# Optimization experiments

Measured on AMD Instinct MI355X. Metric: run time of the kernel, lower is better.

The kernel has to match this reference:

```python
import jax, jax.numpy as jnp
import numpy as np

DEC = 1024
MEM = 1024


def setup_inputs() -> dict:
    key = jax.random.key(0)
    k1, k2, k3, k4, k5 = jax.random.split(key, 5)
    decoder_state = jax.random.normal(k1, (64, DEC), dtype=jnp.float32)
    memory_bank = jax.random.normal(k2, (64, 2048, MEM), dtype=jnp.float32)
    src_mask = jnp.ones((64, 2048), dtype=jnp.int32)
    # learned params (torch Linear: y = x @ W.T); store as (in, out) for einsum
    s = 1.0 / np.sqrt(DEC)
    W_v = jax.random.uniform(k3, (DEC,), jnp.float32, -s, s)            # v: decoder_size -> 1
    W_dec = jax.random.uniform(k4, (DEC, DEC), jnp.float32, -s, s)       # decode_project
    sm = 1.0 / np.sqrt(MEM)
    W_mem = jax.random.uniform(k5, (MEM, DEC), jnp.float32, -sm, sm)     # memory_project
    return {"decoder_state": decoder_state, "memory_bank": memory_bank,
            "src_mask": src_mask, "W_v": W_v, "W_dec": W_dec, "W_mem": W_mem}


def reference(decoder_state, memory_bank, src_mask, W_v, W_dec, W_mem):
    # encoder_feature: [B,S,D]; dec_feature: [B,D]
    enc_feat = jnp.einsum('bsm,md->bsd', memory_bank, W_mem)
    dec_feat = jnp.einsum('bm,md->bd', decoder_state, W_dec)
    e = jnp.tanh(enc_feat + dec_feat[:, None, :])      # [B,S,D]
    scores = jnp.einsum('bsd,d->bs', e, W_v)           # [B,S]
    scores = jnp.where(src_mask == 0, -jnp.inf, scores)
    attn_dist = jax.nn.softmax(scores, axis=-1)        # [B,S]
    context = jnp.einsum('bs,bsm->bm', attn_dist, memory_bank)  # [B,M]
    return (context, attn_dist)
```

## Files before the change

### kernel.cpp

```cpp
#include <hip/hip_runtime.h>

typedef __bf16 bf16;
typedef __bf16 bf16x8 __attribute__((ext_vector_type(8)));
typedef float f32x4 __attribute__((ext_vector_type(4)));

constexpr int kB = 64;
constexpr int kS = 2048;
constexpr int kD = 1024;
constexpr int kM = 1024;
constexpr int kRows = kB * kS;

__device__ __forceinline__ void async_copy16(const void* gsrc, void* ldst) {
    __builtin_amdgcn_global_load_lds(
        (const __attribute__((address_space(1))) void*)gsrc,
        (__attribute__((address_space(3))) void*)ldst, 16, 0, 0);
}

__device__ __forceinline__ float fast_tanh(float x) {
    float e = __expf(2.0f * x);
    return 1.0f - 2.0f * __builtin_amdgcn_rcpf(e + 1.0f);
}

__global__ __launch_bounds__(256) void wmem_transpose_kernel(
    const float* __restrict__ Wm, bf16* __restrict__ WT) {
    __shared__ bf16 tile[64][72];
    const int d0 = (blockIdx.x & 15) * 64;
    const int m0 = (blockIdx.x >> 4) * 64;
    const int lane = threadIdx.x & 63;
    const int grp  = threadIdx.x >> 6;
    #pragma unroll
    for (int r = 0; r < 16; ++r) {
        const int m = m0 + grp * 16 + r;
        tile[lane][grp * 16 + r] = (bf16)Wm[m * 1024 + d0 + lane];
    }
    __syncthreads();
    #pragma unroll
    for (int r = 0; r < 16; ++r) {
        const int d = d0 + grp * 16 + r;
        WT[d * 1024 + m0 + lane] = tile[grp * 16 + r][lane];
    }
}

__global__ __launch_bounds__(256) void dec_project_kernel(
    const float* __restrict__ dec, const float* __restrict__ Wd,
    float* __restrict__ decf) {
    const int b = blockIdx.x;
    const int d = blockIdx.y * 256 + threadIdx.x;
    const float* drow = dec + b * kD;
    float acc = 0.f;
    #pragma unroll 8
    for (int m = 0; m < kM; ++m)
        acc += drow[m] * Wd[(size_t)m * kD + d];
    decf[b * kD + d] = acc;
}

constexpr int BM = 128, BN = 256, BK = 32, APAD = 40;
constexpr int NCOL = kD / BN;
constexpr int NSTEP = kM / BK;

__global__ __launch_bounds__(512, 4) void attn_scores_kernel(
    const float* __restrict__ MBank,
    const bf16*  __restrict__ WT,
    const float* __restrict__ decf,
    const float* __restrict__ Wv,
    float* __restrict__ spart)
{
    __shared__ bf16 Abuf[2][BM * APAD];
    __shared__ bf16 Bbuf[2][BN * BK];
    __shared__ float sred[BM * 4];

    const int tid  = threadIdx.x;
    const int wave = tid >> 6;
    const int lane = tid & 63;
    const int ln   = lane & 15;
    const int quad = lane >> 4;

    const int L = blockIdx.y * NCOL + blockIdx.x;
    const int jw = L >> 3;
    const int rowTile = ((L & 7) << 7) + (jw >> 2);
    const int colTile = jw & 3;
    const int R0 = rowTile * BM;
    const int C0 = colTile * BN;
    const int batch = rowTile >> 4;

    const int wr = (wave >> 2) * 64;
    const int wc = (wave & 3) * 64;

    const int arow  = tid >> 2;
    const int akseg = (tid & 3) * 8;
    const float* aptr = MBank + (size_t)(R0 + arow) * kM + akseg;

    const int bn0   = (lane >> 2);
    const int bkoff = (lane & 3) * 8;

    {
        const float* ap = aptr;
        f32x4 v0 = *(const f32x4*)(ap + 0);
        f32x4 v1 = *(const f32x4*)(ap + 4);
        #pragma unroll
        for (int jj = 0; jj < 2; ++jj) {
            const int chunk = wave * 2 + jj;
            const int n = chunk * 16 + bn0;
            async_copy16(WT + (size_t)(C0 + n) * kM + bkoff,
                         Bbuf[0] + chunk * 512);
        }
        bf16x8 w0;
        w0[0]=(bf16)v0[0]; w0[1]=(bf16)v0[1]; w0[2]=(bf16)v0[2]; w0[3]=(bf16)v0[3];
        w0[4]=(bf16)v1[0]; w0[5]=(bf16)v1[1]; w0[6]=(bf16)v1[2]; w0[7]=(bf16)v1[3];
        *(bf16x8*)(Abuf[0] + arow * APAD + akseg) = w0;
    }
    __syncthreads();

    f32x4 acc[4][4];
    const f32x4 zero = {0.f, 0.f, 0.f, 0.f};
    #pragma unroll
    for (int i = 0; i < 4; ++i)
        #pragma unroll
        for (int j = 0; j < 4; ++j)
            acc[i][j] = zero;

    #pragma unroll 2
    for (int t = 0; t < NSTEP; ++t) {
        const int cur = t & 1, nxt = cur ^ 1;
        const bool pf = (t + 1 < NSTEP);
        const int k1 = (t + 1) * BK;

        f32x4 v0, v1;
        if (pf) {
            const float* ap = aptr + k1;
            v0 = *(const f32x4*)(ap + 0);
            v1 = *(const f32x4*)(ap + 4);
            #pragma unroll
            for (int jj = 0; jj < 2; ++jj) {
                const int chunk = wave * 2 + jj;
                const int n = chunk * 16 + bn0;
                async_copy16(WT + (size_t)(C0 + n) * kM + k1 + bkoff,
                             Bbuf[nxt] + chunk * 512);
            }
        }

        const bf16* Ac = Abuf[cur];
        const bf16* Bc = Bbuf[cur];
        bf16x8 af[4], bfr[4];
        #pragma unroll
        for (int i = 0; i < 4; ++i)
            af[i] = *(const bf16x8*)(Ac + (wr + i * 16 + ln) * APAD + quad * 8);
        #pragma unroll
        for (int j = 0; j < 4; ++j)
            bfr[j] = *(const bf16x8*)(Bc + (wc + j * 16 + ln) * BK + quad * 8);
        __builtin_amdgcn_s_setprio(1);
        #pragma unroll
        for (int i = 0; i < 4; ++i)
            #pragma unroll
            for (int j = 0; j < 4; ++j)
                acc[i][j] = __builtin_amdgcn_mfma_f32_16x16x32_bf16(
                    af[i], bfr[j], acc[i][j], 0, 0, 0);
        __builtin_amdgcn_s_setprio(0);

        if (pf) {
            bf16x8 w0;
            w0[0]=(bf16)v0[0]; w0[1]=(bf16)v0[1]; w0[2]=(bf16)v0[2]; w0[3]=(bf16)v0[3];
            w0[4]=(bf16)v1[0]; w0[5]=(bf16)v1[1]; w0[6]=(bf16)v1[2]; w0[7]=(bf16)v1[3];
            *(bf16x8*)(Abuf[nxt] + arow * APAD + akseg) = w0;
        }
        __syncthreads();
    }

    float wv[4], df[4];
    #pragma unroll
    for (int j = 0; j < 4; ++j) {
        const int d = C0 + wc + j * 16 + ln;
        wv[j] = Wv[d];
        df[j] = decf[batch * kD + d];
    }
    float rp[4][4];
    #pragma unroll
    for (int i = 0; i < 4; ++i) {
        #pragma unroll
        for (int r = 0; r < 4; ++r) {
            float p = 0.f;
            #pragma unroll
            for (int j = 0; j < 4; ++j) {
                float x = acc[i][j][r] + df[j];
                p += fast_tanh(x) * wv[j];
            }
            #pragma unroll
            for (int off = 1; off < 16; off <<= 1)
                p += __shfl_xor(p, off, 64);
            rp[i][r] = p;
        }
    }
    if (ln == 0) {
        #pragma unroll
        for (int i = 0; i < 4; ++i)
            #pragma unroll
            for (int r = 0; r < 4; ++r)
                sred[(wr + i * 16 + quad * 4 + r) * 4 + (wave & 3)] = rp[i][r];
    }
    __syncthreads();
    if (tid < BM)
        spart[(size_t)colTile * kRows + R0 + tid] =
            (sred[tid * 4 + 0] + sred[tid * 4 + 1]) +
            (sred[tid * 4 + 2] + sred[tid * 4 + 3]);
}

__global__ __launch_bounds__(256) void softmax_kernel(
    const float* __restrict__ spart, const int* __restrict__ mask,
    float* __restrict__ attn) {
    const int b = blockIdx.x;
    const int tid = threadIdx.x;
    __shared__ float sc[kS];
    __shared__ float redm[4], reds[4];

    float lmax = -INFINITY;
    for (int s = tid; s < kS; s += 256) {
        float v = 0.f;
        #pragma unroll
        for (int t = 0; t < NCOL; ++t) v += spart[(size_t)t * kRows + b * kS + s];
        if (mask[b * kS + s] == 0) v = -INFINITY;
        sc[s] = v;
        lmax = fmaxf(lmax, v);
    }
    #pragma unroll
    for (int off = 32; off; off >>= 1) lmax = fmaxf(lmax, __shfl_xor(lmax, off, 64));
    if ((tid & 63) == 0) redm[tid >> 6] = lmax;
    __syncthreads();
    const float bmax = fmaxf(fmaxf(redm[0], redm[1]), fmaxf(redm[2], redm[3]));

    float lsum = 0.f;
    for (int s = tid; s < kS; s += 256) {
        float e = __expf(sc[s] - bmax);
        sc[s] = e;
        lsum += e;
    }
    #pragma unroll
    for (int off = 32; off; off >>= 1) lsum += __shfl_xor(lsum, off, 64);
    if ((tid & 63) == 0) reds[tid >> 6] = lsum;
    __syncthreads();
    const float inv = 1.0f / (reds[0] + reds[1] + reds[2] + reds[3]);
    for (int s = tid; s < kS; s += 256) attn[b * kS + s] = sc[s] * inv;
}

__global__ __launch_bounds__(256) void ctx_partial_kernel(
    const float* __restrict__ MBank, const float* __restrict__ attn,
    float* __restrict__ cpart) {
    const int b  = blockIdx.x;
    const int sc = blockIdx.y;
    const int m4 = threadIdx.x * 4;
    const float* base = MBank + ((size_t)b * kS + sc * 128) * kM + m4;
    const float* ap = attn + b * kS + sc * 128;
    f32x4 acc0 = {0.f, 0.f, 0.f, 0.f};
    f32x4 acc1 = {0.f, 0.f, 0.f, 0.f};
    #pragma unroll 4
    for (int s = 0; s < 128; s += 2) {
        const float a0 = ap[s];
        const float a1 = ap[s + 1];
        f32x4 u0 = *(const f32x4*)(base + (size_t)s * kM);
        f32x4 u1 = *(const f32x4*)(base + (size_t)(s + 1) * kM);
        acc0 += u0 * a0;
        acc1 += u1 * a1;
    }
    f32x4 r = acc0 + acc1;
    *(f32x4*)&cpart[((size_t)(b * 16 + sc)) * kM + m4] = r;
}

__global__ __launch_bounds__(256) void ctx_reduce_kernel(
    const float* __restrict__ cpart, float* __restrict__ out) {
    const int idx = blockIdx.x * 256 + threadIdx.x;
    const int b = idx >> 10, m = idx & 1023;
    float v = 0.f;
    #pragma unroll
    for (int c = 0; c < 16; ++c) v += cpart[(size_t)((b * 16 + c) << 10) + m];
    out[idx] = v;
}

extern "C" void kernel_launch(void* const* d_in, const int* in_sizes, int n_in,
                              void* d_out, int out_size, void* d_ws, size_t ws_size,
                              hipStream_t stream) {
    const float* dec   = (const float*)d_in[0];
    const float* MBank = (const float*)d_in[1];
    const int*   mask  = (const int*)d_in[2];
    const float* Wv    = (const float*)d_in[3];
    const float* Wdec  = (const float*)d_in[4];
    const float* Wmem  = (const float*)d_in[5];

    float* out_ctx  = (float*)d_out;
    float* out_attn = (float*)d_out + kB * kD;

    char* ws = (char*)d_ws;
    bf16*  WT    = (bf16*)ws;
    float* decf  = (float*)(ws + (1 << 21));
    float* spart = (float*)(ws + (1 << 21) + (1 << 18));
    float* cpart = (float*)(ws + (1 << 21) + (1 << 18) + (1 << 21));

    wmem_transpose_kernel<<<256, 256, 0, stream>>>(Wmem, WT);
    dec_project_kernel<<<dim3(64, 4), 256, 0, stream>>>(dec, Wdec, decf);
    attn_scores_kernel<<<dim3(NCOL, 1024), 512, 0, stream>>>(MBank, WT, decf, Wv, spart);
    softmax_kernel<<<64, 256, 0, stream>>>(spart, mask, out_attn);
    ctx_partial_kernel<<<dim3(64, 16), 256, 0, stream>>>(MBank, out_attn, cpart);
    ctx_reduce_kernel<<<256, 256, 0, stream>>>(cpart, out_ctx);
}
```

Measured before the change: 1.135 ms.

## Swizzle B LDS tile, alias reduction scratch, raise occupancy, reshape context split

```diff
diff --git a/kernel.cpp b/kernel.cpp
--- a/kernel.cpp
+++ b/kernel.cpp
@@ -58,7 +58,7 @@
 constexpr int NCOL = kD / BN;
 constexpr int NSTEP = kM / BK;
 
-__global__ __launch_bounds__(512, 4) void attn_scores_kernel(
+__global__ __launch_bounds__(512, 6) void attn_scores_kernel(
     const float* __restrict__ MBank,
     const bf16*  __restrict__ WT,
     const float* __restrict__ decf,
@@ -67,7 +67,7 @@
 {
     __shared__ bf16 Abuf[2][BM * APAD];
     __shared__ bf16 Bbuf[2][BN * BK];
-    __shared__ float sred[BM * 4];
+    float* sred = (float*)&Abuf[0][0];
 
     const int tid  = threadIdx.x;
     const int wave = tid >> 6;
@@ -90,8 +90,9 @@
     const int akseg = (tid & 3) * 8;
     const float* aptr = MBank + (size_t)(R0 + arow) * kM + akseg;
 
-    const int bn0   = (lane >> 2);
-    const int bkoff = (lane & 3) * 8;
+    const int bn0  = lane >> 2;
+    const int bsrc = ((lane & 3) ^ ((lane >> 3) & 3)) * 8;
+    const int rswz = (quad ^ ((ln >> 1) & 3)) * 8;
 
     {
         const float* ap = aptr;
@@ -101,7 +102,7 @@
         for (int jj = 0; jj < 2; ++jj) {
             const int chunk = wave * 2 + jj;
             const int n = chunk * 16 + bn0;
-            async_copy16(WT + (size_t)(C0 + n) * kM + bkoff,
+            async_copy16(WT + (size_t)(C0 + n) * kM + bsrc,
                          Bbuf[0] + chunk * 512);
         }
         bf16x8 w0;
@@ -134,7 +135,7 @@
             for (int jj = 0; jj < 2; ++jj) {
                 const int chunk = wave * 2 + jj;
                 const int n = chunk * 16 + bn0;
-                async_copy16(WT + (size_t)(C0 + n) * kM + k1 + bkoff,
+                async_copy16(WT + (size_t)(C0 + n) * kM + k1 + bsrc,
                              Bbuf[nxt] + chunk * 512);
             }
         }
@@ -147,7 +148,7 @@
             af[i] = *(const bf16x8*)(Ac + (wr + i * 16 + ln) * APAD + quad * 8);
         #pragma unroll
         for (int j = 0; j < 4; ++j)
-            bfr[j] = *(const bf16x8*)(Bc + (wc + j * 16 + ln) * BK + quad * 8);
+            bfr[j] = *(const bf16x8*)(Bc + (wc + j * 16 + ln) * BK + rswz);
         __builtin_amdgcn_s_setprio(1);
         #pragma unroll
         for (int i = 0; i < 4; ++i)
@@ -241,27 +242,29 @@
     for (int s = tid; s < kS; s += 256) attn[b * kS + s] = sc[s] * inv;
 }
 
+constexpr int NSC = 8;
+constexpr int SCL = kS / NSC;
+
 __global__ __launch_bounds__(256) void ctx_partial_kernel(
     const float* __restrict__ MBank, const float* __restrict__ attn,
     float* __restrict__ cpart) {
     const int b  = blockIdx.x;
     const int sc = blockIdx.y;
     const int m4 = threadIdx.x * 4;
-    const float* base = MBank + ((size_t)b * kS + sc * 128) * kM + m4;
-    const float* ap = attn + b * kS + sc * 128;
-    f32x4 acc0 = {0.f, 0.f, 0.f, 0.f};
-    f32x4 acc1 = {0.f, 0.f, 0.f, 0.f};
-    #pragma unroll 4
-    for (int s = 0; s < 128; s += 2) {
-        const float a0 = ap[s];
-        const float a1 = ap[s + 1];
-        f32x4 u0 = *(const f32x4*)(base + (size_t)s * kM);
-        f32x4 u1 = *(const f32x4*)(base + (size_t)(s + 1) * kM);
-        acc0 += u0 * a0;
-        acc1 += u1 * a1;
-    }
-    f32x4 r = acc0 + acc1;
-    *(f32x4*)&cpart[((size_t)(b * 16 + sc)) * kM + m4] = r;
+    const float* base = MBank + ((size_t)b * kS + sc * SCL) * kM + m4;
+    const float* ap = attn + b * kS + sc * SCL;
+    f32x4 a0 = {0,0,0,0}, a1 = {0,0,0,0}, a2 = {0,0,0,0}, a3 = {0,0,0,0};
+    #pragma unroll 2
+    for (int s = 0; s < SCL; s += 4) {
+        const float c0 = ap[s], c1 = ap[s+1], c2 = ap[s+2], c3 = ap[s+3];
+        f32x4 u0 = *(const f32x4*)(base + (size_t)(s+0) * kM);
+        f32x4 u1 = *(const f32x4*)(base + (size_t)(s+1) * kM);
+        f32x4 u2 = *(const f32x4*)(base + (size_t)(s+2) * kM);
+        f32x4 u3 = *(const f32x4*)(base + (size_t)(s+3) * kM);
+        a0 += u0 * c0; a1 += u1 * c1; a2 += u2 * c2; a3 += u3 * c3;
+    }
+    f32x4 r = (a0 + a1) + (a2 + a3);
+    *(f32x4*)&cpart[((size_t)(b * NSC + sc)) * kM + m4] = r;
 }
 
 __global__ __launch_bounds__(256) void ctx_reduce_kernel(
@@ -270,7 +273,7 @@
     const int b = idx >> 10, m = idx & 1023;
     float v = 0.f;
     #pragma unroll
-    for (int c = 0; c < 16; ++c) v += cpart[(size_t)((b * 16 + c) << 10) + m];
+    for (int c = 0; c < NSC; ++c) v += cpart[(size_t)((b * NSC + c) << 10) + m];
     out[idx] = v;
 }
 
@@ -297,6 +300,6 @@
     dec_project_kernel<<<dim3(64, 4), 256, 0, stream>>>(dec, Wdec, decf);
     attn_scores_kernel<<<dim3(NCOL, 1024), 512, 0, stream>>>(MBank, WT, decf, Wv, spart);
     softmax_kernel<<<64, 256, 0, stream>>>(spart, mask, out_attn);
-    ctx_partial_kernel<<<dim3(64, 16), 256, 0, stream>>>(MBank, out_attn, cpart);
+    ctx_partial_kernel<<<dim3(64, NSC), 256, 0, stream>>>(MBank, out_attn, cpart);
     ctx_reduce_kernel<<<256, 256, 0, stream>>>(cpart, out_ctx);
 }
```

After: 3.870 ms. 3.41x slower.
